# Optimization experiments

Measured on AMD Instinct MI355X. Metric: run time of the kernel, lower is better.

## Reference

```python
import jax, jax.numpy as jnp
import numpy as np

B, C_IN, N = 64, 64, 4097          # N = T + 1 (index 0 is the null node)
T = N - 1
HID, LAT = 128, 64
EPS = 1e-5


def _tree_conv(trees, children, W, b):
    # trees: (B, C, N); children: (B, 3T) int indices into node axis
    Bn, C, _ = trees.shape
    idx = jnp.broadcast_to(children[:, None, :], (Bn, C, children.shape[1]))
    g = jnp.take_along_axis(trees, idx, axis=2)        # (B, C, 3T) gather
    g = g.reshape(Bn, C, -1, 3)                        # (B, C, T, 3)
    out = jnp.einsum('bctk,ock->bot', g, W) + b[None, :, None]  # (B, O, T)
    zero = jnp.zeros((Bn, out.shape[1], 1), out.dtype)  # null-node column
    return jnp.concatenate([zero, out], axis=2)         # (B, O, T+1)


def _tree_layer_norm(x):
    # normalize over (channels, nodes) per example; torch.std -> ddof=1
    mean = jnp.mean(x, axis=(1, 2), keepdims=True)
    std = jnp.std(x, axis=(1, 2), ddof=1, keepdims=True)
    return (x - mean) / (std + EPS)


def _encode(feats, children, W1, b1, W2, b2):
    x = _tree_conv(feats, children, W1, b1)
    x = jax.nn.relu(_tree_layer_norm(x))
    x = _tree_conv(x, children, W2, b2)
    x = jax.nn.relu(_tree_layer_norm(x))   # dropout is identity in eval
    return jnp.max(x, axis=2)              # DynamicPooling: (B, HID)


def setup_inputs() -> dict:
    key = jax.random.key(0)
    ks = jax.random.split(key, 12)
    s_in = 1.0 / np.sqrt(3 * C_IN)
    s_h = 1.0 / np.sqrt(3 * HID)
    s_fc = 1.0 / np.sqrt(2 * HID)
    return {
        'logical_feats': jax.random.normal(ks[0], (B, C_IN, N), jnp.float32),
        'physical_feats': jax.random.normal(ks[1], (B, C_IN, N), jnp.float32),
        'children': jax.random.randint(ks[2], (B, 3 * T), 0, N, jnp.int32),
        'Wl1': jax.random.normal(ks[3], (HID, C_IN, 3), jnp.float32) * s_in,
        'bl1': jnp.zeros((HID,), jnp.float32),
        'Wl2': jax.random.normal(ks[4], (HID, HID, 3), jnp.float32) * s_h,
        'bl2': jnp.zeros((HID,), jnp.float32),
        'Wp1': jax.random.normal(ks[5], (HID, C_IN, 3), jnp.float32) * s_in,
        'bp1': jnp.zeros((HID,), jnp.float32),
        'Wp2': jax.random.normal(ks[6], (HID, HID, 3), jnp.float32) * s_h,
        'bp2': jnp.zeros((HID,), jnp.float32),
        'Wmu': jax.random.normal(ks[7], (LAT, 2 * HID), jnp.float32) * s_fc,
        'bmu': jnp.zeros((LAT,), jnp.float32),
        'Wlv': jax.random.normal(ks[8], (LAT, 2 * HID), jnp.float32) * s_fc,
        'blv': jnp.zeros((LAT,), jnp.float32),
    }


def reference(logical_feats, physical_feats, children,
              Wl1, bl1, Wl2, bl2, Wp1, bp1, Wp2, bp2,
              Wmu, bmu, Wlv, blv):
    # NOTE: source module passes log_children to BOTH encoders; kept faithful.
    l_embed = _encode(logical_feats, children, Wl1, bl1, Wl2, bl2)
    p_embed = _encode(physical_feats, children, Wp1, bp1, Wp2, bp2)
    combined = jnp.concatenate([l_embed, p_embed], axis=-1)  # (B, 2*HID)
    mu = combined @ Wmu.T + bmu
    logvar = combined @ Wlv.T + blv
    return mu, logvar
```

## Files before the change

kernel.cpp:

```cpp
#include <hip/hip_runtime.h>
#include <hip/hip_bf16.h>

#define NODES 4097
#define TT 4096
#define CIN 64
#define HID 128
#define BATCH 64
#define EPS 1e-5f

typedef short bf16x8 __attribute__((ext_vector_type(8)));
typedef float f32x16 __attribute__((ext_vector_type(16)));

__global__ __launch_bounds__(256) void k_transpose(const float* __restrict__ f0,
                                                   const float* __restrict__ f1,
                                                   __hip_bfloat16* __restrict__ out) {
    __shared__ float tile[32][33];
    int z = blockIdx.z;
    int enc = z >> 6, b = z & 63;
    const float* in = enc ? f1 : f0;
    __hip_bfloat16* o = out + (size_t)enc * BATCH * NODES * CIN;
    int n0 = blockIdx.x * 32;
    int c0 = blockIdx.y * 32;
    int tx = threadIdx.x, ty = threadIdx.y;
    for (int i = 0; i < 32; i += 8) {
        int n = n0 + tx, c = c0 + ty + i;
        float v = 0.f;
        if (n < NODES) v = in[((size_t)b * CIN + c) * NODES + n];
        tile[ty + i][tx] = v;
    }
    __syncthreads();
    for (int i = 0; i < 32; i += 8) {
        int n = n0 + ty + i, c = c0 + tx;
        if (n < NODES) o[((size_t)b * NODES + n) * CIN + c] = __float2bfloat16(tile[tx][ty + i]);
    }
}

__global__ void k_wprep(const float* __restrict__ W0, const float* __restrict__ W1,
                        __hip_bfloat16* __restrict__ Wp, int C) {
    int enc = blockIdx.y;
    const float* W = enc ? W1 : W0;
    __hip_bfloat16* o = Wp + (size_t)enc * 3 * C * HID;
    int id = blockIdx.x * 256 + threadIdx.x;
    int total = 3 * C * HID / 8;
    if (id >= total) return;
    int lane = id & 63;
    int ct = (id >> 6) & 3;
    int ks = id >> 8;
    int n = ct * 32 + (lane & 31);
    int kb = ks * 16 + (lane >> 5) * 8;
    union { int4 i; __hip_bfloat16 h[8]; } u;
#pragma unroll
    for (int j = 0; j < 8; ++j) {
        int k = kb + j;
        int slot = k / C, c = k % C;
        u.h[j] = __float2bfloat16(W[(n * C + c) * 3 + slot]);
    }
    ((int4*)o)[id] = u.i;
}

template <int C, bool POOL>
__global__ __launch_bounds__(256) void k_conv_mfma(
    const __hip_bfloat16* __restrict__ xT,
    const int* __restrict__ children,
    const __hip_bfloat16* __restrict__ Wp,
    const float* __restrict__ bias0, const float* __restrict__ bias1,
    __hip_bfloat16* __restrict__ y,
    float* __restrict__ sums,
    float* __restrict__ pool_part) {
    constexpr int KSc = C / 16;
    constexpr int KS = 3 * KSc;
    int L = blockIdx.x;
    int xcd = L & 7;
    int idx = L >> 3;
    int xt = idx & 31;
    int bg = (idx >> 5) & 7;
    int enc = idx >> 8;
    int b = xcd + 8 * bg;
    const int t0 = xt * 128;
    const int tid = threadIdx.x;
    const int lane = tid & 63;
    const int w = tid >> 6;
    const int hi = lane >> 5;

    const __hip_bfloat16* x = xT + (size_t)enc * BATCH * NODES * C;
    const int4* WpB = (const int4*)(Wp + (size_t)enc * 3 * C * HID);
    const float* bias = enc ? bias1 : bias0;
    const int sb = enc * BATCH + b;
    const size_t rowbase = (size_t)b * NODES;
    const long cb3 = (long)b * (3 * TT);
    const int tnode = t0 + w * 32 + (lane & 31);

    const int4* ap[3];
#pragma unroll
    for (int s = 0; s < 3; ++s) {
        int child = children[cb3 + (long)tnode * 3 + s];
        ap[s] = (const int4*)(x + (rowbase + child) * C) + hi;
    }

    f32x16 acc[4] = {};
#pragma unroll
    for (int ksg = 0; ksg < KS; ++ksg) {
        int slot = ksg / KSc, ksl = ksg % KSc;
        union { int4 i; bf16x8 v; } a;
        a.i = ap[slot][ksl * 2];
#pragma unroll
        for (int cti = 0; cti < 4; ++cti) {
            union { int4 i; bf16x8 v; } bb;
            bb.i = WpB[(ksg * 4 + cti) * 64 + lane];
            acc[cti] = __builtin_amdgcn_mfma_f32_32x32x16_bf16(a.v, bb.v, acc[cti], 0, 0, 0);
        }
    }

    __shared__ float red[512];
    __shared__ float pm[1024];
    float bsum = 0.f, bss = 0.f;
    __hip_bfloat16* yp = POOL ? nullptr : (y + (size_t)enc * BATCH * NODES * HID);
    const int rbase = t0 + w * 32 + 4 * hi + 1;
#pragma unroll
    for (int cti = 0; cti < 4; ++cti) {
        int o = cti * 32 + (lane & 31);
        float bv = bias[o];
        f32x16 a = acc[cti];
        float lmax = -3.4e38f;
#pragma unroll
        for (int reg = 0; reg < 16; ++reg) {
            float v = a[reg] + bv;
            bsum += v;
            bss += v * v;
            if (POOL) {
                lmax = fmaxf(lmax, v);
            } else {
                int row = rbase + (reg & 3) + 8 * (reg >> 2);
                yp[(rowbase + row) * HID + o] = __float2bfloat16(v);
            }
        }
        if (POOL) pm[o * 8 + w * 2 + hi] = lmax;
    }
    if (!POOL && xt == 0 && tid < HID)
        yp[rowbase * HID + tid] = __float2bfloat16(0.f);

    red[tid] = bsum;
    red[256 + tid] = bss;
    __syncthreads();
    for (int s2 = 128; s2 > 0; s2 >>= 1) {
        if (tid < s2) { red[tid] += red[tid + s2]; red[256 + tid] += red[256 + tid + s2]; }
        __syncthreads();
    }
    if (tid == 0) {
        atomicAdd(&sums[sb * 2], red[0]);
        atomicAdd(&sums[sb * 2 + 1], red[256]);
    }
    if (POOL && tid < HID) {
        float m = -3.4e38f;
#pragma unroll
        for (int s2 = 0; s2 < 8; ++s2) m = fmaxf(m, pm[tid * 8 + s2]);
        pool_part[((size_t)sb * 32 + xt) * HID + tid] = m;
    }
}

__global__ void k_stats(const float* __restrict__ sums, float* __restrict__ ms) {
    int s = threadIdx.x;
    const float M = (float)HID * (float)NODES;
    float S = sums[s * 2], SS = sums[s * 2 + 1];
    float mean = S / M;
    float var = (SS - S * S / M) / (M - 1.f);
    float sd = sqrtf(fmaxf(var, 0.f));
    ms[s * 2] = mean;
    ms[s * 2 + 1] = 1.f / (sd + EPS);
}

__global__ __launch_bounds__(256) void k_norm(__hip_bfloat16* __restrict__ y,
                                              const float* __restrict__ ms) {
    constexpr int Q = NODES * HID / 8;
    int s = blockIdx.y;
    int q = blockIdx.x * 256 + threadIdx.x;
    if (q >= Q) return;
    float mean = ms[s * 2], scale = ms[s * 2 + 1];
    int4* p = (int4*)(y + (size_t)s * NODES * HID) + q;
    union { int4 i; __hip_bfloat16 h[8]; } u;
    u.i = *p;
#pragma unroll
    for (int j = 0; j < 8; ++j) {
        float f = (__bfloat162float(u.h[j]) - mean) * scale;
        u.h[j] = __float2bfloat16(f > 0.f ? f : 0.f);
    }
    *p = u.i;
}

__global__ __launch_bounds__(128) void k_pool_fin(const float* __restrict__ part,
                                                  const float* __restrict__ ms1,
                                                  float* __restrict__ combined) {
    int b = blockIdx.x, enc = blockIdx.y, o = threadIdx.x;
    int sb = enc * BATCH + b;
    float m = 0.f;
#pragma unroll 4
    for (int s = 0; s < 32; ++s)
        m = fmaxf(m, part[((size_t)sb * 32 + s) * HID + o]);
    float v = (m - ms1[sb * 2]) * ms1[sb * 2 + 1];
    combined[b * 256 + enc * 128 + o] = v > 0.f ? v : 0.f;
}

__global__ __launch_bounds__(128) void k_fc(const float* __restrict__ combined,
                                            const float* __restrict__ Wmu, const float* __restrict__ bmu,
                                            const float* __restrict__ Wlv, const float* __restrict__ blv,
                                            float* __restrict__ out) {
    int b = blockIdx.x;
    int tid = threadIdx.x;
    __shared__ float cb[256];
    cb[tid] = combined[b * 256 + tid];
    cb[tid + 128] = combined[b * 256 + tid + 128];
    __syncthreads();
    const float* W = (tid < 64) ? Wmu : Wlv;
    int l = tid & 63;
    float s = (tid < 64) ? bmu[l] : blv[l];
    for (int j = 0; j < 256; ++j) s += cb[j] * W[l * 256 + j];
    out[(tid < 64 ? 0 : BATCH * 64) + b * 64 + l] = s;
}

extern "C" void kernel_launch(void* const* d_in, const int* in_sizes, int n_in,
                              void* d_out, int out_size, void* d_ws, size_t ws_size,
                              hipStream_t stream) {
    const int* children = (const int*)d_in[2];
    const float* Wmu = (const float*)d_in[11];
    const float* bmu = (const float*)d_in[12];
    const float* Wlv = (const float*)d_in[13];
    const float* blv = (const float*)d_in[14];

    char* ws = (char*)d_ws;
    size_t off = 0;
    auto alloc = [&](size_t bytes) { void* p = ws + off; off += (bytes + 255) & ~(size_t)255; return p; };
    float* sums = (float*)alloc(2 * 2 * BATCH * 2 * sizeof(float));
    float* msbuf = (float*)alloc(2 * 2 * BATCH * 2 * sizeof(float));
    float* combined = (float*)alloc((size_t)BATCH * 256 * sizeof(float));
    float* pool_part = (float*)alloc((size_t)2 * BATCH * 32 * HID * sizeof(float));
    __hip_bfloat16* Wp1 = (__hip_bfloat16*)alloc((size_t)2 * 3 * CIN * HID * sizeof(__hip_bfloat16));
    __hip_bfloat16* Wp2 = (__hip_bfloat16*)alloc((size_t)2 * 3 * HID * HID * sizeof(__hip_bfloat16));
    __hip_bfloat16* fT = (__hip_bfloat16*)alloc((size_t)2 * BATCH * NODES * CIN * sizeof(__hip_bfloat16));
    __hip_bfloat16* y1 = (__hip_bfloat16*)alloc((size_t)2 * BATCH * NODES * HID * sizeof(__hip_bfloat16));

    hipMemsetAsync(sums, 0, 2 * 2 * BATCH * 2 * sizeof(float), stream);

    k_wprep<<<dim3(3 * CIN * HID / 8 / 256, 2), 256, 0, stream>>>(
        (const float*)d_in[3], (const float*)d_in[7], Wp1, CIN);
    k_wprep<<<dim3(3 * HID * HID / 8 / 256, 2), 256, 0, stream>>>(
        (const float*)d_in[5], (const float*)d_in[9], Wp2, HID);
    k_transpose<<<dim3(129, 2, 2 * BATCH), dim3(32, 8), 0, stream>>>(
        (const float*)d_in[0], (const float*)d_in[1], fT);

    k_conv_mfma<CIN, false><<<4096, 256, 0, stream>>>(
        fT, children, Wp1, (const float*)d_in[4], (const float*)d_in[8], y1, sums, nullptr);
    k_stats<<<1, 128, 0, stream>>>(sums, msbuf);
    k_norm<<<dim3((NODES * HID / 8 + 255) / 256, 2 * BATCH), 256, 0, stream>>>(y1, msbuf);
    k_conv_mfma<HID, true><<<4096, 256, 0, stream>>>(
        y1, children, Wp2, (const float*)d_in[6], (const float*)d_in[10], nullptr,
        sums + 256, pool_part);
    k_stats<<<1, 128, 0, stream>>>(sums + 256, msbuf + 256);
    k_pool_fin<<<dim3(BATCH, 2), 128, 0, stream>>>(pool_part, msbuf + 256, combined);

    k_fc<<<BATCH, 128, 0, stream>>>(combined, Wmu, bmu, Wlv, blv, (float*)d_out);
}
```

Measured before the change: 462.1 us.

## Stage conv weight tiles in LDS via direct global-to-LDS loads

The conv MFMA kernel now copies weight B-fragments into shared memory in phases of 12 k-steps using global_load_lds, instead of having every wave read the same weights from global memory. The four waves share one LDS copy, and the gathered A rows for the phase are prefetched into registers. The reduction and pooling scratch now reuse the weight buffer, and the pool-max layout is transposed to avoid LDS bank conflicts. In exchange it adds per-phase barriers, higher register pressure from the areg array, and a larger LDS footprint that may lower occupancy.

```diff
diff --git a/kernel.cpp b/kernel.cpp
--- a/kernel.cpp
+++ b/kernel.cpp
@@ -10,6 +10,13 @@
 
 typedef short bf16x8 __attribute__((ext_vector_type(8)));
 typedef float f32x16 __attribute__((ext_vector_type(16)));
+
+__device__ __forceinline__ void load_lds16(const void* g, void* l) {
+    __builtin_amdgcn_global_load_lds(
+        (const __attribute__((address_space(1))) unsigned int*)(uintptr_t)g,
+        (__attribute__((address_space(3))) unsigned int*)(uintptr_t)l,
+        16, 0, 0);
+}
 
 __global__ __launch_bounds__(256) void k_transpose(const float* __restrict__ f0,
                                                    const float* __restrict__ f1,
@@ -69,6 +76,8 @@
     float* __restrict__ pool_part) {
     constexpr int KSc = C / 16;
     constexpr int KS = 3 * KSc;
+    constexpr int PK = 12;
+    constexpr int PH = KS / PK;
     int L = blockIdx.x;
     int xcd = L & 7;
     int idx = L >> 3;
@@ -82,6 +91,8 @@
     const int w = tid >> 6;
     const int hi = lane >> 5;
 
+    __shared__ __align__(16) int4 B_lds[PK * 4 * 64];
+
     const __hip_bfloat16* x = xT + (size_t)enc * BATCH * NODES * C;
     const int4* WpB = (const int4*)(Wp + (size_t)enc * 3 * C * HID);
     const float* bias = enc ? bias1 : bias0;
@@ -99,20 +110,36 @@
 
     f32x16 acc[4] = {};
 #pragma unroll
-    for (int ksg = 0; ksg < KS; ++ksg) {
-        int slot = ksg / KSc, ksl = ksg % KSc;
-        union { int4 i; bf16x8 v; } a;
-        a.i = ap[slot][ksl * 2];
-#pragma unroll
-        for (int cti = 0; cti < 4; ++cti) {
-            union { int4 i; bf16x8 v; } bb;
-            bb.i = WpB[(ksg * 4 + cti) * 64 + lane];
-            acc[cti] = __builtin_amdgcn_mfma_f32_32x32x16_bf16(a.v, bb.v, acc[cti], 0, 0, 0);
-        }
-    }
-
-    __shared__ float red[512];
-    __shared__ float pm[1024];
+    for (int ph = 0; ph < PH; ++ph) {
+        if (ph) __syncthreads();
+#pragma unroll
+        for (int i = 0; i < PK; ++i) {
+            int chunk = w * PK + i;
+            load_lds16(WpB + (size_t)(ph * PK * 4 + chunk) * 64 + lane, B_lds + chunk * 64);
+        }
+        int4 areg[PK];
+#pragma unroll
+        for (int kk = 0; kk < PK; ++kk) {
+            int ksg = ph * PK + kk;
+            areg[kk] = ap[ksg / KSc][(ksg % KSc) * 2];
+        }
+        __syncthreads();
+#pragma unroll
+        for (int kk = 0; kk < PK; ++kk) {
+            union { int4 i; bf16x8 v; } a;
+            a.i = areg[kk];
+#pragma unroll
+            for (int cti = 0; cti < 4; ++cti) {
+                union { int4 i; bf16x8 v; } bb;
+                bb.i = B_lds[(kk * 4 + cti) * 64 + lane];
+                acc[cti] = __builtin_amdgcn_mfma_f32_32x32x16_bf16(a.v, bb.v, acc[cti], 0, 0, 0);
+            }
+        }
+    }
+
+    __syncthreads();
+    float* red = (float*)B_lds;
+    float* pm = red + 512;
     float bsum = 0.f, bss = 0.f;
     __hip_bfloat16* yp = POOL ? nullptr : (y + (size_t)enc * BATCH * NODES * HID);
     const int rbase = t0 + w * 32 + 4 * hi + 1;
@@ -134,7 +161,7 @@
                 yp[(rowbase + row) * HID + o] = __float2bfloat16(v);
             }
         }
-        if (POOL) pm[o * 8 + w * 2 + hi] = lmax;
+        if (POOL) pm[(w * 2 + hi) * 128 + o] = lmax;
     }
     if (!POOL && xt == 0 && tid < HID)
         yp[rowbase * HID + tid] = __float2bfloat16(0.f);
@@ -153,7 +180,7 @@
     if (POOL && tid < HID) {
         float m = -3.4e38f;
 #pragma unroll
-        for (int s2 = 0; s2 < 8; ++s2) m = fmaxf(m, pm[tid * 8 + s2]);
+        for (int s2 = 0; s2 < 8; ++s2) m = fmaxf(m, pm[s2 * 128 + tid]);
         pool_part[((size_t)sb * 32 + xt) * HID + tid] = m;
     }
 }
```

Measured after the change: 404.3 us. 12.5% less time.
